# Optimization experiments

Hardware: AMD Instinct MI355X
Metric: run time of the kernel (lower is better)

## Reference

```python
import math
import jax, jax.numpy as jnp
import numpy as np

# ---- config (from ModelConfig) ----
HIDDEN = 2880
HEAD_DIM = 64
N_HEADS = 64
N_KV = 8
Q_MULT = N_HEADS // N_KV  # 8
SLIDING_WINDOW = 128      # left context; causal windowed attention
ROPE_BASE = 150000.0
ROPE_SCALE = 32.0
NTK_ALPHA = 1.0
NTK_BETA = 32.0
INIT_CTX = 4096
RMS_EPS = 1e-5
SM_SCALE = 1.0 / math.sqrt(HEAD_DIM)
Q_DIM = N_HEADS * HEAD_DIM   # 4096
KV_DIM = N_KV * HEAD_DIM     # 512
QKV_DIM = Q_DIM + 2 * KV_DIM # 5120
B, T = 1, 2048


def _rope_cos_sin(n_tokens):
    """YaRN-scaled rotary cache, per RotaryEmbedding._compute_concentration_and_inv_freq."""
    d_half = HEAD_DIM // 2
    freq = ROPE_BASE ** (jnp.arange(0, HEAD_DIM, 2, dtype=jnp.float32) / HEAD_DIM)
    concentration = 0.1 * math.log(ROPE_SCALE) + 1.0
    low = d_half * math.log(INIT_CTX / (NTK_BETA * 2 * math.pi)) / math.log(ROPE_BASE)
    high = d_half * math.log(INIT_CTX / (NTK_ALPHA * 2 * math.pi)) / math.log(ROPE_BASE)
    interpolation = 1.0 / (ROPE_SCALE * freq)
    extrapolation = 1.0 / freq
    ramp = (jnp.arange(d_half, dtype=jnp.float32) - low) / (high - low)
    mask = 1.0 - jnp.clip(ramp, 0.0, 1.0)
    inv_freq = interpolation * (1.0 - mask) + extrapolation * mask
    pos = jnp.arange(n_tokens, dtype=jnp.float32)
    angles = pos[:, None] * inv_freq[None, :]  # [t, d/2]
    return jnp.cos(angles) * concentration, jnp.sin(angles) * concentration


def _apply_rope(x, cos, sin):
    """Interleaved RoPE (matches _apply_rotary_emb). x: [b, t, ..., d]."""
    shape = x.shape
    n_mid = x.ndim - 3  # dims between token axis and feature axis
    c = cos.reshape((1, shape[1]) + (1,) * n_mid + (shape[-1] // 2,))
    s = sin.reshape((1, shape[1]) + (1,) * n_mid + (shape[-1] // 2,))
    x1 = x[..., ::2]
    x2 = x[..., 1::2]
    o1 = x1 * c - x2 * s
    o2 = x2 * c + x1 * s
    return jnp.stack((o1, o2), axis=-1).reshape(shape)


def _rmsnorm(x, scale):
    t = x.astype(jnp.float32)
    t = t * jax.lax.rsqrt(jnp.mean(t * t, axis=-1, keepdims=True) + RMS_EPS)
    return (t * scale).astype(x.dtype)


def setup_inputs() -> dict:
    key = jax.random.key(0)
    ks = jax.random.split(key, 7)
    x = jax.random.normal(ks[0], (B, T, HIDDEN), dtype=jnp.float32)
    norm_scale = jnp.ones((HIDDEN,), dtype=jnp.float32)
    w_qkv = jax.random.normal(ks[1], (QKV_DIM, HIDDEN), dtype=jnp.float32) * (HIDDEN ** -0.5)
    b_qkv = jax.random.normal(ks[2], (QKV_DIM,), dtype=jnp.float32) * 0.02
    sinks = jax.random.normal(ks[3], (N_HEADS,), dtype=jnp.float32)
    w_out = jax.random.normal(ks[4], (HIDDEN, Q_DIM), dtype=jnp.float32) * (Q_DIM ** -0.5)
    b_out = jax.random.normal(ks[5], (HIDDEN,), dtype=jnp.float32) * 0.02
    return {"x": x, "norm_scale": norm_scale, "w_qkv": w_qkv, "b_qkv": b_qkv,
            "sinks": sinks, "w_out": w_out, "b_out": b_out}


def reference(x, norm_scale, w_qkv, b_qkv, sinks, w_out, b_out):
    b, t, _ = x.shape
    h = _rmsnorm(x, norm_scale)
    qkv = h @ w_qkv.T + b_qkv  # [b, t, 5120]
    q = qkv[..., :Q_DIM].reshape(b, t, N_KV, Q_MULT, HEAD_DIM)
    k = qkv[..., Q_DIM:Q_DIM + KV_DIM].reshape(b, t, N_KV, HEAD_DIM)
    v = qkv[..., Q_DIM + KV_DIM:].reshape(b, t, N_KV, HEAD_DIM)

    cos, sin = _rope_cos_sin(t)
    q = _apply_rope(q, cos, sin)
    k = _apply_rope(k, cos, sin)

    # sliding-window causal attention with sink logits (sdpa windowed path)
    left_ctx = SLIDING_WINDOW
    window = left_ctx + 1
    kp = jnp.pad(k, ((0, 0), (left_ctx, 0), (0, 0), (0, 0)))
    vp = jnp.pad(v, ((0, 0), (left_ctx, 0), (0, 0), (0, 0)))
    gather_idx = jnp.arange(t)[:, None] + jnp.arange(window)[None, :]  # into padded axis
    kwin = kp[:, gather_idx]  # [b, t, w, n_kv, d]
    vwin = vp[:, gather_idx]

    pos = jnp.arange(t)[:, None] + (jnp.arange(window) - left_ctx)[None, :]
    valid = (pos >= 0) & (pos < t)  # [t, w]

    scores = jnp.einsum('bthqd,btwhd->bthqw', q, kwin).astype(jnp.float32) * SM_SCALE
    scores = jnp.where(valid[None, :, None, None, :], scores, -jnp.inf)

    sink = (sinks * math.log(2.0)).reshape(N_KV, Q_MULT)
    sink = jnp.broadcast_to(sink[None, None, :, :, None], (b, t, N_KV, Q_MULT, 1))
    scores = jnp.concatenate([scores, sink], axis=-1)  # [b, t, h, q, w+1]

    w_attn = jax.nn.softmax(scores, axis=-1)[..., :-1].astype(v.dtype)
    attn = jnp.einsum('bthqw,btwhd->bthqd', w_attn, vwin).reshape(b, t, -1)

    out = attn @ w_out.T + b_out
    return x + out
```

## Files before the change

kernel.cpp:

```cpp
#include <hip/hip_runtime.h>
#include <math.h>

typedef unsigned short u16;
typedef unsigned int   u32;
using f32x4  = __attribute__((ext_vector_type(4))) float;
using bf16x8 = __attribute__((ext_vector_type(8))) __bf16;

#define HIDDEN   2880
#define QKVD     5120
#define QD       4096
#define TTOK     2048
#define NKV      8
#define QMULT    8
#define HD       64
#define NPAD     2944

#define PREP_QKV_BLOCKS  14400
#define PREP_RMS_BLOCKS  2048

static __device__ __forceinline__ float bflo(u32 u){ return __uint_as_float(u << 16); }
static __device__ __forceinline__ float bfhi(u32 u){ return __uint_as_float(u & 0xffff0000u); }
static __device__ __forceinline__ u16 f2bf(float f){
    u32 u = __float_as_uint(f);
    u32 r = (u + 0x7fffu + ((u >> 16) & 1u)) >> 16;
    return (u16)r;
}

static __device__ __forceinline__ void glds16(const void* g, void* l) {
    __builtin_amdgcn_global_load_lds(
        (__attribute__((address_space(1))) void*)g,
        (__attribute__((address_space(3))) void*)l,
        16, 0, 0);
}

#define BAR() asm volatile("s_barrier" ::: "memory")

__global__ __launch_bounds__(256) void prep_kernel(const float* __restrict__ w_qkv,
                                                   u16* __restrict__ wqkv_bf,
                                                   const float* __restrict__ x,
                                                   const float* __restrict__ scale,
                                                   u16* __restrict__ h) {
    const int b = blockIdx.x;
    const int tid = threadIdx.x;
    if (b < PREP_QKV_BLOCKS) {
        int i = b * 256 + tid;
        float4 f = ((const float4*)w_qkv)[i];
        ushort4 o;
        o.x = f2bf(f.x); o.y = f2bf(f.y); o.z = f2bf(f.z); o.w = f2bf(f.w);
        ((ushort4*)wqkv_bf)[i] = o;
    } else {
        const int t = b - PREP_QKV_BLOCKS;
        const float4* xr = (const float4*)(x + (long)t * HIDDEN);
        float4 v[3];
        float ss = 0.f;
        #pragma unroll
        for (int it = 0; it < 3; ++it) {
            int i4 = tid + it * 256;
            if (i4 < 720) {
                v[it] = xr[i4];
                ss += v[it].x*v[it].x + v[it].y*v[it].y + v[it].z*v[it].z + v[it].w*v[it].w;
            }
        }
        #pragma unroll
        for (int off = 32; off > 0; off >>= 1) ss += __shfl_down(ss, off);
        __shared__ float red[4];
        if ((tid & 63) == 0) red[tid >> 6] = ss;
        __syncthreads();
        float tot = red[0] + red[1] + red[2] + red[3];
        float rr = rsqrtf(tot * (1.0f / HIDDEN) + 1e-5f);
        ushort4* hr = (ushort4*)(h + (long)t * HIDDEN);
        #pragma unroll
        for (int it = 0; it < 3; ++it) {
            int i4 = tid + it * 256;
            if (i4 < 720) {
                float4 s4 = ((const float4*)scale)[i4];
                ushort4 o;
                o.x = f2bf(v[it].x * rr * s4.x);
                o.y = f2bf(v[it].y * rr * s4.y);
                o.z = f2bf(v[it].z * rr * s4.z);
                o.w = f2bf(v[it].w * rr * s4.w);
                hr[i4] = o;
            }
        }
    }
}


#define LOAD_AQ(MH) do { \
    aq[0][0] = *(const bf16x8*)(aS + (2*(MH)+0)*2048 + off0); \
    aq[0][1] = *(const bf16x8*)(aS + (2*(MH)+0)*2048 + off1); \
    aq[1][0] = *(const bf16x8*)(aS + (2*(MH)+1)*2048 + off0); \
    aq[1][1] = *(const bf16x8*)(aS + (2*(MH)+1)*2048 + off1); \
} while (0)

#define MFMA_Q(MH) do { \
    __builtin_amdgcn_s_setprio(1); \
    _Pragma("unroll") \
    for (int i2_ = 0; i2_ < 2; ++i2_) { \
        _Pragma("unroll") \
        for (int ni_ = 0; ni_ < 4; ++ni_) { \
            acc[2*(MH)+i2_][ni_] = __builtin_amdgcn_mfma_f32_16x16x32_bf16(aq[i2_][0], bq[ni_][0], acc[2*(MH)+i2_][ni_], 0, 0, 0); \
            acc[2*(MH)+i2_][ni_] = __builtin_amdgcn_mfma_f32_16x16x32_bf16(aq[i2_][1], bq[ni_][1], acc[2*(MH)+i2_][ni_], 0, 0, 0); \
        } \
    } \
    __builtin_amdgcn_s_setprio(0); \
} while (0)

__global__ __launch_bounds__(512, 2) void gemm_bt_8ph(const u16* __restrict__ A,
                                                      const u16* __restrict__ B,
                                                      u16* __restrict__ C0,
                                                      int N, int K, int ksplit,
                                                      int blimit, int colmax,
                                                      int nz_gemm,
                                                      const float* __restrict__ wout_src,
                                                      u16* __restrict__ wout_dst) {
    const int tid  = threadIdx.x;

    if ((int)blockIdx.z >= nz_gemm) {
        const long nb = (long)gridDim.x * gridDim.y;
        long bidx = (long)blockIdx.y * gridDim.x + blockIdx.x;
        long i = bidx * 512 + tid;
        const long tot = (long)NPAD * QD / 4;
        const long stride = nb * 512;
        for (; i < tot; i += stride) {
            long idx = i * 4;
            int row = (int)(idx >> 12);
            int col = (int)(idx & 4095);
            ushort4 o;
            if (row < HIDDEN) {
                float4 f = *(const float4*)(wout_src + (long)row * QD + col);
                o.x = f2bf(f.x); o.y = f2bf(f.y); o.z = f2bf(f.z); o.w = f2bf(f.w);
            } else {
                o.x = 0; o.y = 0; o.z = 0; o.w = 0;
            }
            ((ushort4*)wout_dst)[i] = o;
        }
        return;
    }

    extern __shared__ u16 smem[];
    u16* const smA = smem;
    u16* const smB = smem + 3 * 256 * 64;
    const int lane = tid & 63;
    const int wv   = tid >> 6;
    const int wm   = wv >> 2;
    const int wn   = wv & 3;
    const long m0  = (long)blockIdx.y * 256;
    const long n0  = (long)blockIdx.x * 256;
    const int kbase = blockIdx.z * ksplit;
    const int NT   = ksplit >> 6;
    u16* C = C0 + (size_t)blockIdx.z * ((size_t)TTOK * N);

    const int srow = tid >> 3;
    const int sg8  = ((tid & 7) ^ (srow & 7)) << 3;
    const int fr   = lane & 15;
    const int off0 = ((lane >> 4) << 4) ^ ((lane & 7) << 4);
    const int off1 = off0 ^ 64;
    const char* aR = (const char*)smA + (wm * 128 + fr) * 128;
    const char* bR = (const char*)smB + (wn * 64  + fr) * 128;

    f32x4 acc[8][4];
    #pragma unroll
    for (int i = 0; i < 8; ++i)
        #pragma unroll
        for (int j = 0; j < 4; ++j) acc[i][j] = f32x4{0.f, 0.f, 0.f, 0.f};

    const u16* Asrc = A + (m0 + srow) * (long)K + kbase + sg8;
    auto stageA = [&](int t, int slot) {
        char* dst = (char*)smA + slot * 32768 + (wv * 8) * 128;
        const u16* src = Asrc + t * 64;
        #pragma unroll
        for (int hj = 0; hj < 4; ++hj)
            glds16(src + (size_t)(hj * 64) * K, dst + hj * 64 * 128);
    };
    auto stageB = [&](int t, int h) {
        char* dst = (char*)smB + (t & 1) * 32768 + (h * 128 + wv * 8) * 128;
        #pragma unroll
        for (int j = 0; j < 2; ++j) {
            long r = n0 + h * 128 + j * 64 + srow;
            if (r > blimit) r = blimit;
            glds16(B + (size_t)r * K + kbase + t * 64 + sg8, dst + j * 64 * 128);
        }
    };

    stageA(0, 0);
    stageB(0, 0); stageB(0, 1);
    if (NT > 1) { stageA(1, 1); stageB(1, 0); stageB(1, 1); }
    if (NT > 1) asm volatile("s_waitcnt vmcnt(8)" ::: "memory");
    else        asm volatile("s_waitcnt vmcnt(0)" ::: "memory");
    BAR();

    int sA = 0;
    for (int t = 0; t < NT; ++t) {
        const char* aS = aR + sA * 32768;
        const char* bS = bR + (t & 1) * 32768;
        int sA2 = sA + 2; if (sA2 >= 3) sA2 -= 3;
        bf16x8 bq[4][2], aq[2][2];
        #pragma unroll
        for (int ni = 0; ni < 4; ++ni) {
            bq[ni][0] = *(const bf16x8*)(bS + ni * 2048 + off0);
            bq[ni][1] = *(const bf16x8*)(bS + ni * 2048 + off1);
        }
        LOAD_AQ(0);
        if (t + 2 < NT) stageA(t + 2, sA2);
        BAR();
        MFMA_Q(0);
        BAR();
        LOAD_AQ(1);
        if (t + 2 < NT) stageB(t + 2, 0);
        BAR();
        MFMA_Q(1);
        BAR();
        LOAD_AQ(2);
        if (t + 2 < NT) stageB(t + 2, 1);
        BAR();
        MFMA_Q(2);
        BAR();
        LOAD_AQ(3);
        BAR();
        MFMA_Q(3);
        if (t + 2 < NT)      asm volatile("s_waitcnt vmcnt(8)" ::: "memory");
        else if (t + 1 < NT) asm volatile("s_waitcnt vmcnt(0)" ::: "memory");
        BAR();
        sA = (sA == 2) ? 0 : sA + 1;
    }

    const int cr = (lane >> 4) * 4;
    const int cc = lane & 15;
    #pragma unroll
    for (int ni = 0; ni < 4; ++ni) {
        long col = n0 + wn * 64 + ni * 16 + cc;
        if (col < colmax) {
            #pragma unroll
            for (int mi = 0; mi < 8; ++mi) {
                long row = m0 + wm * 128 + mi * 16 + cr;
                #pragma unroll
                for (int r2 = 0; r2 < 4; ++r2)
                    C[(row + r2) * (long)N + col] = f2bf(acc[mi][ni][r2]);
            }
        }
    }
}

__global__ __launch_bounds__(256) void rope_kernel(const u16* __restrict__ p1,
                                                   const float* __restrict__ b_qkv,
                                                   u16* __restrict__ qr,
                                                   u16* __restrict__ kr,
                                                   u16* __restrict__ vr) {
    const int t = blockIdx.x;
    const int tid = threadIdx.x;
    __shared__ float cs[32], sn[32];
    if (tid < 32) {
        float fi = (float)tid;
        float freq   = exp2f(17.1946032f * (fi * (1.0f / 32.0f)));
        float interp = 1.0f / (32.0f * freq);
        float extra  = 1.0f / freq;
        float ramp   = (fi - 8.0927802f) * (1.0f / (17.3980220f - 8.0927802f));
        float rc     = fminf(fmaxf(ramp, 0.0f), 1.0f);
        float invf   = interp * rc + extra * (1.0f - rc);
        float ang    = (float)t * invf;
        cs[tid] = cosf(ang) * 1.3465736f;
        sn[tid] = sinf(ang) * 1.3465736f;
    }
    __syncthreads();
    const u16* rowA = p1 + (long)t * QKVD;
    auto pair = [&](int col) -> float2 {
        u32 ua = *(const u32*)(rowA + col);
        float2 bb = *(const float2*)(b_qkv + col);
        return make_float2(bflo(ua) + bb.x, bfhi(ua) + bb.y);
    };
    for (int p = tid; p < 2048; p += 256) {
        int hd2 = p >> 5, i = p & 31;
        float2 ab = pair(hd2 * 64 + 2 * i);
        float o1 = ab.x * cs[i] - ab.y * sn[i];
        float o2 = ab.y * cs[i] + ab.x * sn[i];
        *(u32*)(qr + (long)t * QD + hd2 * 64 + 2 * i) = (u32)f2bf(o1) | ((u32)f2bf(o2) << 16);
    }
    {
        int kv = tid >> 5, i = tid & 31;
        float2 ab = pair(QD + kv * 64 + 2 * i);
        float o1 = ab.x * cs[i] - ab.y * sn[i];
        float o2 = ab.y * cs[i] + ab.x * sn[i];
        *(u32*)(kr + ((long)kv * TTOK + t) * HD + 2 * i) = (u32)f2bf(o1) | ((u32)f2bf(o2) << 16);
    }
    {
        int kv = tid >> 5, d2 = tid & 31;
        float2 ab = pair(QD + 512 + kv * 64 + 2 * d2);
        *(u32*)(vr + ((long)kv * TTOK + t) * HD + 2 * d2) = (u32)f2bf(ab.x) | ((u32)f2bf(ab.y) << 16);
    }
}

__global__ __launch_bounds__(256, 2) void attn_kernel(const u16* __restrict__ qr,
                                                      const u16* __restrict__ kr,
                                                      const u16* __restrict__ vr,
                                                      const float* __restrict__ sinks,
                                                      u16* __restrict__ o) {
    const int t0  = blockIdx.x * 16;
    const int h   = blockIdx.y;
    const int qhg = blockIdx.z;
    const int tid = threadIdx.x;
    const int lane = tid & 63, wv = tid >> 6;
    __shared__ __align__(16) u16 ks[144][72];
    __shared__ __align__(16) u16 Vt[64][168];
    __shared__ __align__(16) u16 P [4][16][168];
    const u16* kb = kr + (long)h * TTOK * HD;
    const u16* vb = vr + (long)h * TTOK * HD;

    #pragma unroll
    for (int i = 0; i < 5; ++i) {
        int idx = i * 256 + tid;
        if (idx < 144 * 8) {
            int rr = idx >> 3, c = idx & 7;
            int tk = t0 - 128 + rr;
            int tks = tk < 0 ? 0 : tk;
            *(uint4*)&ks[rr][c * 8] = *(const uint4*)(kb + (long)tks * HD + c * 8);
        }
    }
    #pragma unroll
    for (int c4 = 0; c4 < 8; ++c4) {
        if (tid < 144) {
            int tk = t0 - 128 + tid;
            int tks = tk < 0 ? 0 : tk;
            uint4 v4 = *(const uint4*)(vb + (long)tks * HD + c4 * 8);
            int d0 = c4 * 8;
            Vt[d0+0][tid] = (u16)(v4.x & 0xffff); Vt[d0+1][tid] = (u16)(v4.x >> 16);
            Vt[d0+2][tid] = (u16)(v4.y & 0xffff); Vt[d0+3][tid] = (u16)(v4.y >> 16);
            Vt[d0+4][tid] = (u16)(v4.z & 0xffff); Vt[d0+5][tid] = (u16)(v4.z >> 16);
            Vt[d0+6][tid] = (u16)(v4.w & 0xffff); Vt[d0+7][tid] = (u16)(v4.w >> 16);
        }
    }
    if (tid < 128) {
        *(uint4*)&Vt[tid >> 1][144 + (tid & 1) * 8] = uint4{0, 0, 0, 0};
    }
    if (lane < 32) {
        *(uint4*)&P[wv][lane >> 1][144 + (lane & 1) * 8] = uint4{0, 0, 0, 0};
    }
    __syncthreads();

    const int qh   = qhg * 4 + wv;
    const int head = h * QMULT + qh;
    const int fr = lane & 15, fk = (lane >> 4) * 8;
    const int cr = (lane >> 4) * 4;

    const u16* qrow = qr + (long)(t0 + fr) * QD + head * HD;
    bf16x8 qf0 = *(const bf16x8*)(qrow + fk);
    bf16x8 qf1 = *(const bf16x8*)(qrow + 32 + fk);

    const int kmin = 128 - t0;
    float lsum[4] = {0.f, 0.f, 0.f, 0.f};

    for (int nt = 0; nt < 9; ++nt) {
        bf16x8 b0 = *(const bf16x8*)&ks[nt * 16 + fr][fk];
        bf16x8 b1 = *(const bf16x8*)&ks[nt * 16 + fr][32 + fk];
        f32x4 s = f32x4{0.f, 0.f, 0.f, 0.f};
        s = __builtin_amdgcn_mfma_f32_16x16x32_bf16(qf0, b0, s, 0, 0, 0);
        s = __builtin_amdgcn_mfma_f32_16x16x32_bf16(qf1, b1, s, 0, 0, 0);
        const int kk = nt * 16 + fr;
        #pragma unroll
        for (int r = 0; r < 4; ++r) {
            int row = cr + r;
            bool valid = (kk >= row) && (kk <= row + 128) && (kk >= kmin);
            float p = valid ? __expf(s[r] * 0.125f) : 0.0f;
            lsum[r] += p;
            P[wv][row][kk] = f2bf(p);
        }
    }

    f32x4 oacc[4];
    #pragma unroll
    for (int dt = 0; dt < 4; ++dt) oacc[dt] = f32x4{0.f, 0.f, 0.f, 0.f};
    #pragma unroll
    for (int k5 = 0; k5 < 5; ++k5) {
        const int k0 = k5 * 32;
        bf16x8 pa = *(const bf16x8*)&P[wv][fr][k0 + fk];
        #pragma unroll
        for (int dt = 0; dt < 4; ++dt) {
            bf16x8 vf = *(const bf16x8*)&Vt[dt * 16 + fr][k0 + fk];
            oacc[dt] = __builtin_amdgcn_mfma_f32_16x16x32_bf16(pa, vf, oacc[dt], 0, 0, 0);
        }
    }

    #pragma unroll
    for (int r = 0; r < 4; ++r) {
        float v = lsum[r];
        v += __shfl_xor(v, 1);
        v += __shfl_xor(v, 2);
        v += __shfl_xor(v, 4);
        v += __shfl_xor(v, 8);
        lsum[r] = v;
    }
    const float sk = exp2f(sinks[head]);
    float inv[4];
    #pragma unroll
    for (int r = 0; r < 4; ++r) inv[r] = 1.0f / (lsum[r] + sk);

    #pragma unroll
    for (int dt = 0; dt < 4; ++dt) {
        #pragma unroll
        for (int r = 0; r < 4; ++r) {
            o[(long)(t0 + cr + r) * QD + head * HD + dt * 16 + fr] = f2bf(oacc[dt][r] * inv[r]);
        }
    }
}

__global__ __launch_bounds__(256) void reduce2_kernel(const u16* __restrict__ p2a,
                                                      const u16* __restrict__ p2b,
                                                      const float* __restrict__ x,
                                                      const float* __restrict__ b_out,
                                                      float* __restrict__ out) {
    const int row = blockIdx.y;
    const int c4 = blockIdx.x * 256 + threadIdx.x;
    if (c4 >= 720) return;
    const int col = c4 * 4;
    ushort4 ua = *(const ushort4*)(p2a + (long)row * NPAD + col);
    ushort4 ub = *(const ushort4*)(p2b + (long)row * NPAD + col);
    float4 xv = *(const float4*)(x + (long)row * HIDDEN + col);
    float4 bv = *(const float4*)(b_out + col);
    float4 o;
    o.x = xv.x + bv.x + __uint_as_float((u32)ua.x << 16) + __uint_as_float((u32)ub.x << 16);
    o.y = xv.y + bv.y + __uint_as_float((u32)ua.y << 16) + __uint_as_float((u32)ub.y << 16);
    o.z = xv.z + bv.z + __uint_as_float((u32)ua.z << 16) + __uint_as_float((u32)ub.z << 16);
    o.w = xv.w + bv.w + __uint_as_float((u32)ua.w << 16) + __uint_as_float((u32)ub.w << 16);
    *(float4*)(out + (long)row * HIDDEN + col) = o;
}

extern "C" void kernel_launch(void* const* d_in, const int* in_sizes, int n_in,
                              void* d_out, int out_size, void* d_ws, size_t ws_size,
                              hipStream_t stream) {
    const float* x      = (const float*)d_in[0];
    const float* nscale = (const float*)d_in[1];
    const float* w_qkv  = (const float*)d_in[2];
    const float* b_qkv  = (const float*)d_in[3];
    const float* sinks  = (const float*)d_in[4];
    const float* w_out  = (const float*)d_in[5];
    const float* b_out  = (const float*)d_in[6];
    float* out = (float*)d_out;

    static int smem_set = 0;
    if (!smem_set) {
        hipFuncSetAttribute((const void*)gemm_bt_8ph,
                            hipFuncAttributeMaxDynamicSharedMemorySize, 163840);
        smem_set = 1;
    }

    char* ws = (char*)d_ws;
    size_t off = 0;
    auto alloc = [&](size_t bytes) { void* p = ws + off; off += (bytes + 255) & ~(size_t)255; return p; };
    u16* wqkv_bf = (u16*)alloc((size_t)QKVD * HIDDEN * 2);
    u16* wout_bf = (u16*)alloc((size_t)NPAD * QD * 2);
    u16* h       = (u16*)alloc((size_t)TTOK * HIDDEN * 2);
    u16* p1      = (u16*)alloc((size_t)2 * TTOK * QKVD * 2);
    u16* qrot    = (u16*)alloc((size_t)TTOK * QD * 2);
    u16* krot    = (u16*)alloc((size_t)NKV * TTOK * HD * 2);
    u16* vrot    = (u16*)alloc((size_t)NKV * TTOK * HD * 2);
    u16* attn = wqkv_bf;
    u16* p2   = p1;

    prep_kernel<<<PREP_QKV_BLOCKS + PREP_RMS_BLOCKS, 256, 0, stream>>>(
        w_qkv, wqkv_bf, x, nscale, h);
    gemm_bt_8ph<<<dim3(QKVD / 256, TTOK / 256, 2), 512, 163840, stream>>>(
        h, wqkv_bf, p1, QKVD, HIDDEN, HIDDEN, QKVD - 1, QKVD, 1, w_out, wout_bf);
    rope_kernel<<<TTOK, 256, 0, stream>>>(p1, b_qkv, qrot, krot, vrot);
    attn_kernel<<<dim3(TTOK / 16, NKV, 2), 256, 0, stream>>>(qrot, krot, vrot, sinks, attn);
    gemm_bt_8ph<<<dim3((NPAD + 255) / 256, TTOK / 256, 2), 512, 163840, stream>>>(
        attn, wout_bf, p2, NPAD, QD, QD / 2, NPAD - 1, NPAD, 2, nullptr, nullptr);
    reduce2_kernel<<<dim3(3, TTOK), 256, 0, stream>>>(
        p2, p2 + (size_t)TTOK * NPAD, x, b_out, out);
}
```

Measured before the change: 334.3 us.

## Restructure GEMM warp tiling to 4x2 with double-buffered A and ping-pong B fragments

Changes the GEMM wave layout from 2x4 (128x64 per wave) to 4x2 (64x128 per wave). Each wave now keeps all A fragments in registers and streams B fragments in alternating register sets. A shared-memory staging drops from triple to double buffering, which reduces dynamic LDS from 160KB to 128KB. The loads for the next tile are issued during the last MFMA phase to overlap LDS reads with compute. The schedule is more complex and relies on tighter vmcnt waits, which risks stalls or hazards.

```diff
diff --git a/kernel.cpp b/kernel.cpp
--- a/kernel.cpp
+++ b/kernel.cpp
@@ -86,21 +86,29 @@
 }
 
 
-#define LOAD_AQ(MH) do { \
-    aq[0][0] = *(const bf16x8*)(aS + (2*(MH)+0)*2048 + off0); \
-    aq[0][1] = *(const bf16x8*)(aS + (2*(MH)+0)*2048 + off1); \
-    aq[1][0] = *(const bf16x8*)(aS + (2*(MH)+1)*2048 + off0); \
-    aq[1][1] = *(const bf16x8*)(aS + (2*(MH)+1)*2048 + off1); \
+#define READ_BQ(SET, BASE, NQ) do { \
+    SET[0][0] = *(const bf16x8*)((BASE) + (2*(NQ)+0)*2048 + off0); \
+    SET[0][1] = *(const bf16x8*)((BASE) + (2*(NQ)+0)*2048 + off1); \
+    SET[1][0] = *(const bf16x8*)((BASE) + (2*(NQ)+1)*2048 + off0); \
+    SET[1][1] = *(const bf16x8*)((BASE) + (2*(NQ)+1)*2048 + off1); \
 } while (0)
 
-#define MFMA_Q(MH) do { \
+#define READ_AQ(BASE) do { \
+    _Pragma("unroll") \
+    for (int mi_ = 0; mi_ < 4; ++mi_) { \
+        aq[mi_][0] = *(const bf16x8*)((BASE) + mi_*2048 + off0); \
+        aq[mi_][1] = *(const bf16x8*)((BASE) + mi_*2048 + off1); \
+    } \
+} while (0)
+
+#define MFMA_N(NQ, SET) do { \
     __builtin_amdgcn_s_setprio(1); \
     _Pragma("unroll") \
-    for (int i2_ = 0; i2_ < 2; ++i2_) { \
+    for (int mi_ = 0; mi_ < 4; ++mi_) { \
         _Pragma("unroll") \
-        for (int ni_ = 0; ni_ < 4; ++ni_) { \
-            acc[2*(MH)+i2_][ni_] = __builtin_amdgcn_mfma_f32_16x16x32_bf16(aq[i2_][0], bq[ni_][0], acc[2*(MH)+i2_][ni_], 0, 0, 0); \
-            acc[2*(MH)+i2_][ni_] = __builtin_amdgcn_mfma_f32_16x16x32_bf16(aq[i2_][1], bq[ni_][1], acc[2*(MH)+i2_][ni_], 0, 0, 0); \
+        for (int j_ = 0; j_ < 2; ++j_) { \
+            acc[mi_][2*(NQ)+j_] = __builtin_amdgcn_mfma_f32_16x16x32_bf16(aq[mi_][0], SET[j_][0], acc[mi_][2*(NQ)+j_], 0, 0, 0); \
+            acc[mi_][2*(NQ)+j_] = __builtin_amdgcn_mfma_f32_16x16x32_bf16(aq[mi_][1], SET[j_][1], acc[mi_][2*(NQ)+j_], 0, 0, 0); \
         } \
     } \
     __builtin_amdgcn_s_setprio(0); \
@@ -140,11 +148,11 @@
 
     extern __shared__ u16 smem[];
     u16* const smA = smem;
-    u16* const smB = smem + 3 * 256 * 64;
+    u16* const smB = smem + 2 * 256 * 64;
     const int lane = tid & 63;
     const int wv   = tid >> 6;
-    const int wm   = wv >> 2;
-    const int wn   = wv & 3;
+    const int wm2  = wv >> 1;
+    const int wn2  = wv & 1;
     const long m0  = (long)blockIdx.y * 256;
     const long n0  = (long)blockIdx.x * 256;
     const int kbase = blockIdx.z * ksplit;
@@ -156,87 +164,91 @@
     const int fr   = lane & 15;
     const int off0 = ((lane >> 4) << 4) ^ ((lane & 7) << 4);
     const int off1 = off0 ^ 64;
-    const char* aR = (const char*)smA + (wm * 128 + fr) * 128;
-    const char* bR = (const char*)smB + (wn * 64  + fr) * 128;
-
-    f32x4 acc[8][4];
-    #pragma unroll
-    for (int i = 0; i < 8; ++i)
-        #pragma unroll
-        for (int j = 0; j < 4; ++j) acc[i][j] = f32x4{0.f, 0.f, 0.f, 0.f};
+    const char* aR = (const char*)smA + (wm2 * 64  + fr) * 128;
+    const char* bR = (const char*)smB + (wn2 * 128 + fr) * 128;
+
+    f32x4 acc[4][8];
+    #pragma unroll
+    for (int i = 0; i < 4; ++i)
+        #pragma unroll
+        for (int j = 0; j < 8; ++j) acc[i][j] = f32x4{0.f, 0.f, 0.f, 0.f};
 
     const u16* Asrc = A + (m0 + srow) * (long)K + kbase + sg8;
-    auto stageA = [&](int t, int slot) {
-        char* dst = (char*)smA + slot * 32768 + (wv * 8) * 128;
+    auto stageA = [&](int t) {
+        char* dst = (char*)smA + (t & 1) * 32768 + wv * 1024;
         const u16* src = Asrc + t * 64;
         #pragma unroll
         for (int hj = 0; hj < 4; ++hj)
-            glds16(src + (size_t)(hj * 64) * K, dst + hj * 64 * 128);
+            glds16(src + (size_t)(hj * 64) * K, dst + hj * 8192);
     };
-    auto stageB = [&](int t, int h) {
+    auto stageBh = [&](int t, int h) {
         char* dst = (char*)smB + (t & 1) * 32768 + (h * 128 + wv * 8) * 128;
         #pragma unroll
         for (int j = 0; j < 2; ++j) {
             long r = n0 + h * 128 + j * 64 + srow;
             if (r > blimit) r = blimit;
-            glds16(B + (size_t)r * K + kbase + t * 64 + sg8, dst + j * 64 * 128);
+            glds16(B + (size_t)r * K + kbase + t * 64 + sg8, dst + j * 8192);
         }
     };
 
-    stageA(0, 0);
-    stageB(0, 0); stageB(0, 1);
-    if (NT > 1) { stageA(1, 1); stageB(1, 0); stageB(1, 1); }
-    if (NT > 1) asm volatile("s_waitcnt vmcnt(8)" ::: "memory");
-    else        asm volatile("s_waitcnt vmcnt(0)" ::: "memory");
+    bf16x8 aq[4][2], bqE[2][2], bqO[2][2];
+
+    stageA(0);
+    stageBh(0, 0); stageBh(0, 1);
+    if (NT > 1) {
+        stageA(1);
+        asm volatile("s_waitcnt vmcnt(4)" ::: "memory");
+        stageBh(1, 0);
+    } else {
+        asm volatile("s_waitcnt vmcnt(0)" ::: "memory");
+    }
     BAR();
-
-    int sA = 0;
+    READ_BQ(bqE, bR, 0);
+    READ_AQ(aR);
+    BAR();
+
     for (int t = 0; t < NT; ++t) {
-        const char* aS = aR + sA * 32768;
-        const char* bS = bR + (t & 1) * 32768;
-        int sA2 = sA + 2; if (sA2 >= 3) sA2 -= 3;
-        bf16x8 bq[4][2], aq[2][2];
-        #pragma unroll
-        for (int ni = 0; ni < 4; ++ni) {
-            bq[ni][0] = *(const bf16x8*)(bS + ni * 2048 + off0);
-            bq[ni][1] = *(const bf16x8*)(bS + ni * 2048 + off1);
-        }
-        LOAD_AQ(0);
-        if (t + 2 < NT) stageA(t + 2, sA2);
-        BAR();
-        MFMA_Q(0);
-        BAR();
-        LOAD_AQ(1);
-        if (t + 2 < NT) stageB(t + 2, 0);
-        BAR();
-        MFMA_Q(1);
-        BAR();
-        LOAD_AQ(2);
-        if (t + 2 < NT) stageB(t + 2, 1);
-        BAR();
-        MFMA_Q(2);
-        BAR();
-        LOAD_AQ(3);
-        BAR();
-        MFMA_Q(3);
-        if (t + 2 < NT)      asm volatile("s_waitcnt vmcnt(8)" ::: "memory");
+        const char* aS1 = aR + ((t + 1) & 1) * 32768;
+        const char* bS  = bR + (t & 1) * 32768;
+        const char* bS1 = bR + ((t + 1) & 1) * 32768;
+        READ_BQ(bqO, bS, 1);
+        if (t + 1 < NT) stageBh(t + 1, 1);
+        if (t + 2 < NT) stageA(t + 2);
+        BAR();
+        MFMA_N(0, bqE);
+        BAR();
+        READ_BQ(bqE, bS, 2);
+        BAR();
+        MFMA_N(1, bqO);
+        BAR();
+        READ_BQ(bqO, bS, 3);
+        BAR();
+        MFMA_N(2, bqE);
+        BAR();
+        if (t + 2 < NT)      asm volatile("s_waitcnt vmcnt(4)" ::: "memory");
         else if (t + 1 < NT) asm volatile("s_waitcnt vmcnt(0)" ::: "memory");
-        BAR();
-        sA = (sA == 2) ? 0 : sA + 1;
+        if (t + 2 < NT) stageBh(t + 2, 0);
+        BAR();
+        MFMA_N(3, bqO);
+        if (t + 1 < NT) {
+            READ_BQ(bqE, bS1, 0);
+            READ_AQ(aS1);
+        }
+        BAR();
     }
 
     const int cr = (lane >> 4) * 4;
     const int cc = lane & 15;
     #pragma unroll
-    for (int ni = 0; ni < 4; ++ni) {
-        long col = n0 + wn * 64 + ni * 16 + cc;
+    for (int nf = 0; nf < 8; ++nf) {
+        long col = n0 + wn2 * 128 + nf * 16 + cc;
         if (col < colmax) {
             #pragma unroll
-            for (int mi = 0; mi < 8; ++mi) {
-                long row = m0 + wm * 128 + mi * 16 + cr;
+            for (int mi = 0; mi < 4; ++mi) {
+                long row = m0 + wm2 * 64 + mi * 16 + cr;
                 #pragma unroll
                 for (int r2 = 0; r2 < 4; ++r2)
-                    C[(row + r2) * (long)N + col] = f2bf(acc[mi][ni][r2]);
+                    C[(row + r2) * (long)N + col] = f2bf(acc[mi][nf][r2]);
             }
         }
     }
@@ -439,7 +451,7 @@
     static int smem_set = 0;
     if (!smem_set) {
         hipFuncSetAttribute((const void*)gemm_bt_8ph,
-                            hipFuncAttributeMaxDynamicSharedMemorySize, 163840);
+                            hipFuncAttributeMaxDynamicSharedMemorySize, 131072);
         smem_set = 1;
     }
 
@@ -458,11 +470,11 @@
 
     prep_kernel<<<PREP_QKV_BLOCKS + PREP_RMS_BLOCKS, 256, 0, stream>>>(
         w_qkv, wqkv_bf, x, nscale, h);
-    gemm_bt_8ph<<<dim3(QKVD / 256, TTOK / 256, 2), 512, 163840, stream>>>(
+    gemm_bt_8ph<<<dim3(QKVD / 256, TTOK / 256, 2), 512, 131072, stream>>>(
         h, wqkv_bf, p1, QKVD, HIDDEN, HIDDEN, QKVD - 1, QKVD, 1, w_out, wout_bf);
     rope_kernel<<<TTOK, 256, 0, stream>>>(p1, b_qkv, qrot, krot, vrot);
     attn_kernel<<<dim3(TTOK / 16, NKV, 2), 256, 0, stream>>>(qrot, krot, vrot, sinks, attn);
-    gemm_bt_8ph<<<dim3((NPAD + 255) / 256, TTOK / 256, 2), 512, 163840, stream>>>(
+    gemm_bt_8ph<<<dim3((NPAD + 255) / 256, TTOK / 256, 2), 512, 131072, stream>>>(
         attn, wout_bf, p2, NPAD, QD, QD / 2, NPAD - 1, NPAD, 2, nullptr, nullptr);
     reduce2_kernel<<<dim3(3, TTOK), 256, 0, stream>>>(
         p2, p2 + (size_t)TTOK * NPAD, x, b_out, out);
```

New measurement: 337.5 us. About the same (+1.0%).
